# Kernel optimization log

Measured on AMD Instinct MI355X. Metric: run time of the kernel, lower is better.

## Reference

```python
import jax, jax.numpy as jnp
import numpy as np

N, IN, H, OUT = 8192, 128, 256, 128

def _xavier(key, shape):
    lim = float(np.sqrt(6.0 / (shape[0] + shape[1])))
    return jax.random.uniform(key, shape, jnp.float32, -lim, lim)

def setup_inputs() -> dict:
    key = jax.random.key(0)
    ks = jax.random.split(key, 9)
    x = jax.random.normal(ks[0], (N, IN), jnp.float32)
    weighted_adj = jax.random.uniform(ks[1], (N, N), jnp.float32)  # positive edge weights
    W1 = _xavier(ks[2], (IN, H))
    W2 = _xavier(ks[3], (H, H))
    W3 = _xavier(ks[4], (H, OUT))
    q = jax.random.normal(ks[5], (OUT, 1), jnp.float32)
    Wl = _xavier(ks[6], (OUT, OUT))  # nn.Linear weight [out, in]
    bl = jnp.zeros((OUT,), jnp.float32)  # nn.Linear bias (torch default init omitted; zeros)
    b = jax.random.normal(ks[7], (1,), jnp.float32)
    return {"x": x, "weighted_adj": weighted_adj, "W1": W1, "W2": W2, "W3": W3,
            "Wl": Wl, "bl": bl, "q": q, "b": b}

def reference(x, weighted_adj, W1, W2, W3, Wl, bl, q, b):
    # D^{-1/2} A D^{-1/2}: broadcast row/col scaling instead of diag matmuls (same math)
    d_inv_sqrt = jnp.sum(weighted_adj, axis=1) ** -0.5  # [N]
    nadj = d_inv_sqrt[:, None] * weighted_adj * d_inv_sqrt[None, :]  # [N, N]
    # 3 stacked GCN layers (normalized adj is identical each layer)
    h = jax.nn.relu(nadj @ (x @ W1))   # [N, H]
    h = jax.nn.relu(nadj @ (h @ W2))   # [N, H]
    z_context = nadj @ (h @ W3)        # [N, OUT]
    # attention pooling: softmax(tanh(z W^T + b_l) q + b) over nodes
    attn_scores = jnp.tanh(z_context @ Wl.T + bl) @ q + b  # [N, 1]
    attn = jax.nn.softmax(attn_scores, axis=0)
    global_context = jnp.sum(attn * z_context, axis=0)  # [OUT]
    return (z_context, global_context)
```

## Files before the change

kernel.cpp:

```cpp
#include <hip/hip_runtime.h>

typedef unsigned short u16;
typedef unsigned int   u32;
typedef __bf16 bf16x8 __attribute__((ext_vector_type(8)));
typedef float  f32x16 __attribute__((ext_vector_type(16)));

__device__ __forceinline__ u16 f2bf(float f){
  u32 u = __float_as_uint(f);
  u32 r = (u + 0x7FFFu + ((u >> 16) & 1u)) >> 16;
  return (u16)r;
}


__global__ __launch_bounds__(1024) void rowsum_tileA(
    const float* __restrict__ A, u16* __restrict__ Ab, float* __restrict__ ds){
  __shared__ u16 lt[8192];
  const int t = threadIdx.x;
  const int r = t >> 5, q = t & 31;
  const int rg = blockIdx.x;
  const float* ar = A + ((size_t)rg * 32 + r) * 8192;
  float s = 0.f;
  for (int ch = 0; ch < 32; ++ch){
    #pragma unroll
    for (int j = 0; j < 2; ++j){
      const int c4 = ch * 64 + j * 32 + q;
      float4 v = ((const float4*)ar)[c4];
      s += (v.x + v.y) + (v.z + v.w);
      const int cl = (j * 32 + q) * 4;
      const int tile = cl >> 4;
      const int tl   = (r | (((cl >> 3) & 1) << 5)) ^ (tile & 7);
      const int idx  = tile * 512 + tl * 8 + (cl & 7);
      ushort4 o;
      o.x = f2bf(v.x); o.y = f2bf(v.y); o.z = f2bf(v.z); o.w = f2bf(v.w);
      *(ushort4*)(lt + idx) = o;
    }
    __syncthreads();
    {
      const int tile = t >> 6, tl = t & 63;
      uint4 v = *(const uint4*)(lt + tile * 512 + (tl ^ (tile & 7)) * 8);
      uint4* dst = (uint4*)(Ab + ((size_t)rg * 512 + ch * 16) * 512);
      dst[t] = v;
    }
    __syncthreads();
  }
  #pragma unroll
  for (int m = 16; m > 0; m >>= 1) s += __shfl_xor(s, m, 64);
  if (q == 0) ds[rg * 32 + r] = rsqrtf(s);
}

template<int K, int F>
__global__ __launch_bounds__(256) void small_gemm(
    const float* __restrict__ inp, const float* __restrict__ W,
    const float* __restrict__ ds, u16* __restrict__ Vt){
  constexpr int RPB = 16;
  __shared__ float xs[RPB * K];
  const int t  = threadIdx.x;
  const int r0 = blockIdx.x * RPB;
  const float* ip = inp + (size_t)r0 * K;
  constexpr int IT = (RPB * K) / (256 * 4);
  #pragma unroll
  for (int j = 0; j < IT; ++j){
    int c = j * 256 + t;
    ((float4*)xs)[c] = ((const float4*)ip)[c];
  }
  __syncthreads();
  const int o = t % F;
  float acc[16];
  #pragma unroll
  for (int r = 0; r < 16; ++r) acc[r] = 0.f;
  for (int k = 0; k < K; k += 4){
    float w0 = W[(k+0)*F + o];
    float w1 = W[(k+1)*F + o];
    float w2 = W[(k+2)*F + o];
    float w3 = W[(k+3)*F + o];
    #pragma unroll
    for (int r = 0; r < 16; ++r){
      float4 xv = *(const float4*)(xs + r*K + k);
      acc[r] += xv.x*w0 + xv.y*w1 + xv.z*w2 + xv.w*w3;
    }
  }
  const int rb = r0;
  union { u16 u[16]; uint4 v[2]; } pk;
  #pragma unroll
  for (int r = 0; r < 16; ++r) pk.u[r] = f2bf(acc[r] * ds[rb + r]);
  const size_t tile = ((size_t)(o >> 5) * 512 + (rb >> 4)) * 512;
  uint4* dst = (uint4*)(Vt + tile + (size_t)(o & 31) * 8);
  dst[0]  = pk.v[0];
  dst[32] = pk.v[1];
}

__global__ __launch_bounds__(64) void prep_w(
    const float* __restrict__ W2, const float* __restrict__ W3,
    u16* __restrict__ W2t, u16* __restrict__ W3t){
  const int b = blockIdx.x, l = threadIdx.x;
  const float* W; u16* Wt; int F, fi;
  if (b < 128){ W = W2; Wt = W2t; F = 256; fi = b; }
  else        { W = W3; Wt = W3t; F = 128; fi = b - 128; }
  const int CT = F / 32;
  const int kt = fi / CT, ct = fi % CT;
  const int o  = ct * 32 + (l & 31);
  const int kb = kt * 16 + (l >> 5) * 8;
  union { u16 u[8]; uint4 v; } pk;
  #pragma unroll
  for (int e = 0; e < 8; ++e) pk.u[e] = f2bf(W[(size_t)(kb + e) * F + o]);
  *(uint4*)(Wt + (size_t)fi * 512 + l * 8) = pk.v;
}

template<int F>
__global__ __launch_bounds__(256) void small_mfma(
    const u16* __restrict__ Ht, const u16* __restrict__ Wt,
    const float* __restrict__ ds, u16* __restrict__ Vt){
  constexpr int CT = F / 128;
  const int t = threadIdx.x, w = t >> 6, lane = t & 63;
  const int rowt = blockIdx.x;
  const u16* ha = Ht + ((size_t)rowt * 16) * 512 + lane * 8;
  const u16* wb = Wt + ((size_t)(w * CT)) * 512 + lane * 8;
  f32x16 acc[CT];
  #pragma unroll
  for (int ct = 0; ct < CT; ++ct)
    #pragma unroll
    for (int i = 0; i < 16; ++i) acc[ct][i] = 0.f;
  #pragma unroll
  for (int kt = 0; kt < 16; ++kt){
    bf16x8 a = *(const bf16x8*)(const void*)(ha + (size_t)kt * 512);
    #pragma unroll
    for (int ct = 0; ct < CT; ++ct){
      bf16x8 b = *(const bf16x8*)(const void*)(wb + (size_t)(kt * (F/32) + ct) * 512);
      acc[ct] = __builtin_amdgcn_mfma_f32_32x32x16_bf16(a, b, acc[ct], 0, 0, 0);
    }
  }
  const int rhi = (lane >> 5) << 2, cl = lane & 31;
  #pragma unroll
  for (int ct = 0; ct < CT; ++ct){
    const size_t obase = ((size_t)(w * CT + ct) * 512 + rowt * 2) * 512;
    #pragma unroll
    for (int r = 0; r < 16; ++r){
      const int rl = (r & 3) + ((r >> 2) << 3) + rhi;
      const int i  = rowt * 32 + rl;
      const u16 v = f2bf(acc[ct][r] * ds[i]);
      Vt[obase + (size_t)(rl >> 4) * 512 + (cl | (((rl >> 3) & 1) << 5)) * 8 + (rl & 7)] = v;
    }
  }
}

__global__ __launch_bounds__(256) void gemm_rt(
    const u16* __restrict__ Ab, const u16* __restrict__ Vt,
    const float* __restrict__ ds, u16* __restrict__ Hout){
  __shared__ u16 Ls[2][32 * 512];
  const int t = threadIdx.x, w = t >> 6, lane = t & 63;
  const int rowg = blockIdx.x & 127;
  const int colg = blockIdx.x >> 7;

  const u16* sP0 = Ab + ((size_t)(rowg * 2 + 0) * 512) * 512 + lane * 8;
  const u16* sP1 = Ab + ((size_t)(rowg * 2 + 1) * 512) * 512 + lane * 8;
  const u16* sP2 = Vt + ((size_t)(colg * 2 + 0) * 512) * 512 + lane * 8;
  const u16* sP3 = Vt + ((size_t)(colg * 2 + 1) * 512) * 512 + lane * 8;

  f32x16 a00, a01, a10, a11;
  #pragma unroll
  for (int i = 0; i < 16; ++i){ a00[i]=0.f; a01[i]=0.f; a10[i]=0.f; a11[i]=0.f; }

  auto stage = [&](int buf, int c){
    u16* L = &Ls[buf][0] + lane * 8;
    #pragma unroll
    for (int h = 0; h < 2; ++h){
      const int kt = c * 8 + h * 4 + w;
      const int sl = h * 4 + w;
      const size_t so = (size_t)kt * 512;
      __builtin_amdgcn_global_load_lds(
        (const __attribute__((address_space(1))) u32*)(sP0 + so),
        (__attribute__((address_space(3))) u32*)(L + (0  + sl) * 512), 16, 0, 0);
      __builtin_amdgcn_global_load_lds(
        (const __attribute__((address_space(1))) u32*)(sP1 + so),
        (__attribute__((address_space(3))) u32*)(L + (8  + sl) * 512), 16, 0, 0);
      __builtin_amdgcn_global_load_lds(
        (const __attribute__((address_space(1))) u32*)(sP2 + so),
        (__attribute__((address_space(3))) u32*)(L + (16 + sl) * 512), 16, 0, 0);
      __builtin_amdgcn_global_load_lds(
        (const __attribute__((address_space(1))) u32*)(sP3 + so),
        (__attribute__((address_space(3))) u32*)(L + (24 + sl) * 512), 16, 0, 0);
    }
  };
  auto compute = [&](int buf){
    const u16* L = &Ls[buf][0] + lane * 8;
    #pragma unroll
    for (int h = 0; h < 2; ++h){
      const int sl = h * 4 + w;
      bf16x8 fa0 = *(const bf16x8*)(const void*)(L + (0  + sl) * 512);
      bf16x8 fa1 = *(const bf16x8*)(const void*)(L + (8  + sl) * 512);
      bf16x8 fb0 = *(const bf16x8*)(const void*)(L + (16 + sl) * 512);
      bf16x8 fb1 = *(const bf16x8*)(const void*)(L + (24 + sl) * 512);
      a00 = __builtin_amdgcn_mfma_f32_32x32x16_bf16(fa0, fb0, a00, 0, 0, 0);
      a01 = __builtin_amdgcn_mfma_f32_32x32x16_bf16(fa0, fb1, a01, 0, 0, 0);
      a10 = __builtin_amdgcn_mfma_f32_32x32x16_bf16(fa1, fb0, a10, 0, 0, 0);
      a11 = __builtin_amdgcn_mfma_f32_32x32x16_bf16(fa1, fb1, a11, 0, 0, 0);
    }
  };

  stage(0, 0);
  __syncthreads();
  for (int c = 0; c < 64; ++c){
    if (c < 63) stage((c + 1) & 1, c + 1);
    compute(c & 1);
    __syncthreads();
  }

  float* Rf = (float*)(&Ls[0][0]);
  f32x16 aq[4];
  aq[0] = a00; aq[1] = a01; aq[2] = a10; aq[3] = a11;
  if (w >= 2){
    float* o = Rf + (w - 2) * 4096 + lane;
    #pragma unroll
    for (int q = 0; q < 4; ++q)
      #pragma unroll
      for (int r = 0; r < 16; ++r)
        o[(q * 16 + r) * 64] = aq[q][r];
  }
  __syncthreads();
  if (w < 2){
    const float* o = Rf + w * 4096 + lane;
    #pragma unroll
    for (int q = 0; q < 4; ++q)
      #pragma unroll
      for (int r = 0; r < 16; ++r)
        aq[q][r] += o[(q * 16 + r) * 64];
  }
  __syncthreads();
  if (w == 1){
    float* o = Rf + lane;
    #pragma unroll
    for (int q = 0; q < 4; ++q)
      #pragma unroll
      for (int r = 0; r < 16; ++r)
        o[(q * 16 + r) * 64] = aq[q][r];
  }
  __syncthreads();
  if (w == 0){
    const float* o = Rf + lane;
    const int rhi = (lane >> 5) << 2;
    const int cl  = lane & 31;
    #pragma unroll
    for (int q = 0; q < 4; ++q){
      const int rowtile = rowg * 2 + (q >> 1);
      const int ct16    = colg * 4 + (q & 1) * 2 + (cl >> 4);
      #pragma unroll
      for (int r = 0; r < 16; ++r){
        const int rl = (r & 3) + ((r >> 2) << 3) + rhi;
        const int row = rowg * 64 + (q >> 1) * 32 + rl;
        float v = aq[q][r] + o[(q * 16 + r) * 64];
        v *= ds[row];
        v = fmaxf(v, 0.f);
        Hout[((size_t)rowtile * 16 + ct16) * 512
             + (rl | (((cl >> 3) & 1) << 5)) * 8 + (cl & 7)] = f2bf(v);
      }
    }
  }
}

__global__ __launch_bounds__(256) void gemm_rt128(
    const u16* __restrict__ Ab, const u16* __restrict__ Vt,
    const float* __restrict__ ds, float* __restrict__ Fout){
  __shared__ u16 Ls[2][24 * 512];
  const int t = threadIdx.x, w = t >> 6, lane = t & 63;
  const int rowg = blockIdx.x & 255;
  const int colg = blockIdx.x >> 8;

  const u16* sA  = Ab + ((size_t)rowg * 512) * 512 + lane * 8;
  const u16* sB0 = Vt + ((size_t)(colg * 2 + 0) * 512) * 512 + lane * 8;
  const u16* sB1 = Vt + ((size_t)(colg * 2 + 1) * 512) * 512 + lane * 8;

  f32x16 p0, p1;
  #pragma unroll
  for (int i = 0; i < 16; ++i){ p0[i] = 0.f; p1[i] = 0.f; }

  auto stage = [&](int buf, int c){
    u16* L = &Ls[buf][0] + lane * 8;
    #pragma unroll
    for (int h = 0; h < 2; ++h){
      const int kt = c * 8 + h * 4 + w;
      const int sl = h * 4 + w;
      const size_t so = (size_t)kt * 512;
      __builtin_amdgcn_global_load_lds(
        (const __attribute__((address_space(1))) u32*)(sA + so),
        (__attribute__((address_space(3))) u32*)(L + (0  + sl) * 512), 16, 0, 0);
      __builtin_amdgcn_global_load_lds(
        (const __attribute__((address_space(1))) u32*)(sB0 + so),
        (__attribute__((address_space(3))) u32*)(L + (8  + sl) * 512), 16, 0, 0);
      __builtin_amdgcn_global_load_lds(
        (const __attribute__((address_space(1))) u32*)(sB1 + so),
        (__attribute__((address_space(3))) u32*)(L + (16 + sl) * 512), 16, 0, 0);
    }
  };
  auto compute = [&](int buf){
    const u16* L = &Ls[buf][0] + lane * 8;
    #pragma unroll
    for (int h = 0; h < 2; ++h){
      const int sl = h * 4 + w;
      bf16x8 fa  = *(const bf16x8*)(const void*)(L + (0  + sl) * 512);
      bf16x8 fb0 = *(const bf16x8*)(const void*)(L + (8  + sl) * 512);
      bf16x8 fb1 = *(const bf16x8*)(const void*)(L + (16 + sl) * 512);
      p0 = __builtin_amdgcn_mfma_f32_32x32x16_bf16(fa, fb0, p0, 0, 0, 0);
      p1 = __builtin_amdgcn_mfma_f32_32x32x16_bf16(fa, fb1, p1, 0, 0, 0);
    }
  };

  stage(0, 0);
  __syncthreads();
  for (int c = 0; c < 64; ++c){
    if (c < 63) stage((c + 1) & 1, c + 1);
    compute(c & 1);
    __syncthreads();
  }

  float* Rf = (float*)(&Ls[0][0]);
  f32x16 aq[2];
  aq[0] = p0; aq[1] = p1;
  if (w >= 2){
    float* o = Rf + (w - 2) * 2048 + lane;
    #pragma unroll
    for (int q = 0; q < 2; ++q)
      #pragma unroll
      for (int r = 0; r < 16; ++r)
        o[(q * 16 + r) * 64] = aq[q][r];
  }
  __syncthreads();
  if (w < 2){
    const float* o = Rf + w * 2048 + lane;
    #pragma unroll
    for (int q = 0; q < 2; ++q)
      #pragma unroll
      for (int r = 0; r < 16; ++r)
        aq[q][r] += o[(q * 16 + r) * 64];
  }
  __syncthreads();
  if (w == 1){
    float* o = Rf + lane;
    #pragma unroll
    for (int q = 0; q < 2; ++q)
      #pragma unroll
      for (int r = 0; r < 16; ++r)
        o[(q * 16 + r) * 64] = aq[q][r];
  }
  __syncthreads();
  if (w == 0){
    const float* o = Rf + lane;
    const int rhi = (lane >> 5) << 2;
    const int cl  = lane & 31;
    #pragma unroll
    for (int q = 0; q < 2; ++q){
      const int cbase = colg * 64 + q * 32;
      #pragma unroll
      for (int r = 0; r < 16; ++r){
        const int rl = (r & 3) + ((r >> 2) << 3) + rhi;
        const int row = rowg * 32 + rl;
        float v = aq[q][r] + o[(q * 16 + r) * 64];
        Fout[(size_t)row * 128 + cbase + cl] = v * ds[row];
      }
    }
  }
}

__device__ __forceinline__ float tanh_fast(float x){
  x = fminf(fmaxf(x, -15.f), 15.f);
  float e = __expf(2.f * x);
  return (e - 1.f) / (e + 1.f);
}

__global__ __launch_bounds__(256) void attn_scores(
    const float* __restrict__ Z, const float* __restrict__ Wl,
    const float* __restrict__ bl, const float* __restrict__ q,
    const float* __restrict__ bsc, float* __restrict__ sc){
  __shared__ float wl[128 * 128];
  const int t = threadIdx.x, lane = t & 63, wave = t >> 6;
  for (int j = 0; j < 64; ++j){
    int idx = j * 256 + t;
    int o = idx >> 7, k = idx & 127;
    int c = k >> 2, e = k & 3;
    wl[o * 128 + (((c ^ (o & 31)) << 2) | e)] = Wl[idx];
  }
  __syncthreads();
  const float bl0 = bl[lane], bl1 = bl[lane + 64];
  const float q0  = q[lane],  q1  = q[lane + 64];
  const float bb  = bsc[0];
  const int r0 = blockIdx.x * 16;
  for (int rr = 0; rr < 4; ++rr){
    int r = r0 + wave * 4 + rr;
    float d0 = 0.f, d1 = 0.f;
    #pragma unroll
    for (int c = 0; c < 32; ++c){
      float4 zv = *(const float4*)(Z + (size_t)r * 128 + c * 4);
      float4 w0 = *(const float4*)&wl[ lane      * 128 + ((c ^ (lane & 31)) << 2)];
      float4 w1 = *(const float4*)&wl[(lane + 64)* 128 + ((c ^ (lane & 31)) << 2)];
      d0 += zv.x*w0.x + zv.y*w0.y + zv.z*w0.z + zv.w*w0.w;
      d1 += zv.x*w1.x + zv.y*w1.y + zv.z*w1.z + zv.w*w1.w;
    }
    float s = tanh_fast(d0 + bl0) * q0 + tanh_fast(d1 + bl1) * q1;
    #pragma unroll
    for (int off = 32; off > 0; off >>= 1) s += __shfl_down(s, off, 64);
    if (lane == 0) sc[r] = s + bb;
  }
}

__global__ __launch_bounds__(1024) void softmax_red(
    const float* __restrict__ sc, float* __restrict__ sred){
  const int t = threadIdx.x, lane = t & 63, wave = t >> 6;
  __shared__ float red[16];
  float m = -1e30f;
  for (int i = t; i < 8192; i += 1024) m = fmaxf(m, sc[i]);
  #pragma unroll
  for (int off = 32; off > 0; off >>= 1) m = fmaxf(m, __shfl_down(m, off, 64));
  if (lane == 0) red[wave] = m;
  __syncthreads();
  if (t == 0){
    float mm = red[0];
    for (int w = 1; w < 16; ++w) mm = fmaxf(mm, red[w]);
    red[0] = mm;
  }
  __syncthreads();
  const float bmax = red[0];
  __syncthreads();
  float s = 0.f;
  for (int i = t; i < 8192; i += 1024) s += __expf(sc[i] - bmax);
  #pragma unroll
  for (int off = 32; off > 0; off >>= 1) s += __shfl_down(s, off, 64);
  if (lane == 0) red[wave] = s;
  __syncthreads();
  if (t == 0){
    float ss = 0.f;
    for (int w = 0; w < 16; ++w) ss += red[w];
    sred[0] = bmax; sred[1] = ss;
  }
}

__global__ __launch_bounds__(256) void weighted_part(
    const float* __restrict__ sc, const float* __restrict__ sred,
    const float* __restrict__ Z, float* __restrict__ part){
  const int blk = blockIdx.x, t = threadIdx.x;
  const int o = t & 127, h = t >> 7;
  const float bmax = sred[0], inv = 1.f / sred[1];
  float acc = 0.f;
  const int i0 = blk * 128;
  for (int i = i0 + h; i < i0 + 128; i += 2){
    float w = __expf(sc[i] - bmax) * inv;
    acc += w * Z[(size_t)i * 128 + o];
  }
  __shared__ float l[256];
  l[t] = acc;
  __syncthreads();
  if (h == 0) part[blk * 128 + o] = l[o] + l[o + 128];
}

__global__ __launch_bounds__(128) void final_red(
    const float* __restrict__ part, float* __restrict__ out){
  const int o = threadIdx.x;
  float s = 0.f;
  for (int b = 0; b < 64; ++b) s += part[b * 128 + o];
  out[o] = s;
}

extern "C" void kernel_launch(void* const* d_in, const int* in_sizes, int n_in,
                              void* d_out, int out_size, void* d_ws, size_t ws_size,
                              hipStream_t stream){
  const float* x  = (const float*)d_in[0];
  const float* A  = (const float*)d_in[1];
  const float* W1 = (const float*)d_in[2];
  const float* W2 = (const float*)d_in[3];
  const float* W3 = (const float*)d_in[4];
  const float* Wl = (const float*)d_in[5];
  const float* bl = (const float*)d_in[6];
  const float* q  = (const float*)d_in[7];
  const float* b  = (const float*)d_in[8];
  float* out = (float*)d_out;
  char* ws = (char*)d_ws;

  u16*   AB   = (u16*)(ws);
  float* DS   = (float*)(ws + 134217728);
  u16*   VT   = (u16*)(ws + 134250496);
  u16*   HB   = (u16*)(ws + 138444800);
  float* SC   = (float*)(ws + 142639104);
  float* SP   = (float*)(ws + 142671872);
  float* SRED = (float*)(ws + 142704640);
  u16*   W2T  = (u16*)(ws + 142705664);
  u16*   W3T  = (u16*)(ws + 142836736);

  rowsum_tileA<<<256, 1024, 0, stream>>>(A, AB, DS);
  prep_w<<<192, 64, 0, stream>>>(W2, W3, W2T, W3T);
  small_gemm<128, 256><<<512, 256, 0, stream>>>(x, W1, DS, VT);
  gemm_rt<<<512, 256, 0, stream>>>(AB, VT, DS, HB);
  small_mfma<256><<<256, 256, 0, stream>>>(HB, W2T, DS, VT);
  gemm_rt<<<512, 256, 0, stream>>>(AB, VT, DS, HB);
  small_mfma<128><<<256, 256, 0, stream>>>(HB, W3T, DS, VT);
  gemm_rt128<<<512, 256, 0, stream>>>(AB, VT, DS, out);
  attn_scores<<<512, 256, 0, stream>>>(out, Wl, bl, q, b, SC);
  softmax_red<<<1, 1024, 0, stream>>>(SC, SRED);
  weighted_part<<<64, 256, 0, stream>>>(SC, SRED, out, SP);
  final_red<<<1, 128, 0, stream>>>(SP, out + 8192 * 128);
}
```

Measured before the change: 307.9 us.

## Use MFMA for first layer x@W1 and double-buffer LDS in rowsum_tileA

The scalar fp32 small_gemm for x@W1 is replaced by a bf16 pack of x (prep_x), a tiled pack of W1 added to prep_w, and the existing MFMA small_mfma kernel templated on K-tile count. The rowsum_tileA kernel double-buffers its LDS staging tile so the second barrier per chunk can be dropped. This trades one fp32 layer for bf16 precision and adds a kernel launch. The main cost it targets is the scalar FMA work and the per-chunk barrier stall.

```diff
diff --git a/kernel.cpp b/kernel.cpp
--- a/kernel.cpp
+++ b/kernel.cpp
@@ -14,13 +14,14 @@
 
 __global__ __launch_bounds__(1024) void rowsum_tileA(
     const float* __restrict__ A, u16* __restrict__ Ab, float* __restrict__ ds){
-  __shared__ u16 lt[8192];
+  __shared__ u16 lt[2][8192];
   const int t = threadIdx.x;
   const int r = t >> 5, q = t & 31;
   const int rg = blockIdx.x;
   const float* ar = A + ((size_t)rg * 32 + r) * 8192;
   float s = 0.f;
   for (int ch = 0; ch < 32; ++ch){
+    u16* lb = lt[ch & 1];
     #pragma unroll
     for (int j = 0; j < 2; ++j){
       const int c4 = ch * 64 + j * 32 + q;
@@ -32,70 +33,51 @@
       const int idx  = tile * 512 + tl * 8 + (cl & 7);
       ushort4 o;
       o.x = f2bf(v.x); o.y = f2bf(v.y); o.z = f2bf(v.z); o.w = f2bf(v.w);
-      *(ushort4*)(lt + idx) = o;
+      *(ushort4*)(lb + idx) = o;
     }
     __syncthreads();
     {
       const int tile = t >> 6, tl = t & 63;
-      uint4 v = *(const uint4*)(lt + tile * 512 + (tl ^ (tile & 7)) * 8);
+      uint4 v = *(const uint4*)(lb + tile * 512 + (tl ^ (tile & 7)) * 8);
       uint4* dst = (uint4*)(Ab + ((size_t)rg * 512 + ch * 16) * 512);
       dst[t] = v;
     }
-    __syncthreads();
   }
   #pragma unroll
   for (int m = 16; m > 0; m >>= 1) s += __shfl_xor(s, m, 64);
   if (q == 0) ds[rg * 32 + r] = rsqrtf(s);
 }
 
-template<int K, int F>
-__global__ __launch_bounds__(256) void small_gemm(
-    const float* __restrict__ inp, const float* __restrict__ W,
-    const float* __restrict__ ds, u16* __restrict__ Vt){
-  constexpr int RPB = 16;
-  __shared__ float xs[RPB * K];
-  const int t  = threadIdx.x;
-  const int r0 = blockIdx.x * RPB;
-  const float* ip = inp + (size_t)r0 * K;
-  constexpr int IT = (RPB * K) / (256 * 4);
-  #pragma unroll
-  for (int j = 0; j < IT; ++j){
-    int c = j * 256 + t;
-    ((float4*)xs)[c] = ((const float4*)ip)[c];
-  }
-  __syncthreads();
-  const int o = t % F;
-  float acc[16];
-  #pragma unroll
-  for (int r = 0; r < 16; ++r) acc[r] = 0.f;
-  for (int k = 0; k < K; k += 4){
-    float w0 = W[(k+0)*F + o];
-    float w1 = W[(k+1)*F + o];
-    float w2 = W[(k+2)*F + o];
-    float w3 = W[(k+3)*F + o];
-    #pragma unroll
-    for (int r = 0; r < 16; ++r){
-      float4 xv = *(const float4*)(xs + r*K + k);
-      acc[r] += xv.x*w0 + xv.y*w1 + xv.z*w2 + xv.w*w3;
-    }
-  }
-  const int rb = r0;
-  union { u16 u[16]; uint4 v[2]; } pk;
-  #pragma unroll
-  for (int r = 0; r < 16; ++r) pk.u[r] = f2bf(acc[r] * ds[rb + r]);
-  const size_t tile = ((size_t)(o >> 5) * 512 + (rb >> 4)) * 512;
-  uint4* dst = (uint4*)(Vt + tile + (size_t)(o & 31) * 8);
-  dst[0]  = pk.v[0];
-  dst[32] = pk.v[1];
+__global__ __launch_bounds__(1024) void prep_x(
+    const float* __restrict__ x, u16* __restrict__ Xt){
+  __shared__ u16 lt[4096];
+  const int t = threadIdx.x;
+  const int r = t >> 5, q = t & 31;
+  const int rg = blockIdx.x;
+  float4 v = ((const float4*)(x + ((size_t)rg * 32 + r) * 128))[q];
+  const int cl = q * 4;
+  const int tile = cl >> 4;
+  const int tl   = (r | (((cl >> 3) & 1) << 5)) ^ (tile & 7);
+  ushort4 o;
+  o.x = f2bf(v.x); o.y = f2bf(v.y); o.z = f2bf(v.z); o.w = f2bf(v.w);
+  *(ushort4*)(lt + tile * 512 + tl * 8 + (cl & 7)) = o;
+  __syncthreads();
+  if (t < 512){
+    const int tile2 = t >> 6, tl2 = t & 63;
+    uint4 w = *(const uint4*)(lt + tile2 * 512 + (tl2 ^ (tile2 & 7)) * 8);
+    ((uint4*)(Xt + (size_t)rg * 4096))[t] = w;
+  }
 }
 
 __global__ __launch_bounds__(64) void prep_w(
-    const float* __restrict__ W2, const float* __restrict__ W3,
+    const float* __restrict__ W1, const float* __restrict__ W2,
+    const float* __restrict__ W3, u16* __restrict__ W1t,
     u16* __restrict__ W2t, u16* __restrict__ W3t){
   const int b = blockIdx.x, l = threadIdx.x;
   const float* W; u16* Wt; int F, fi;
-  if (b < 128){ W = W2; Wt = W2t; F = 256; fi = b; }
-  else        { W = W3; Wt = W3t; F = 128; fi = b - 128; }
+  if (b < 64)       { W = W1; Wt = W1t; F = 256; fi = b; }
+  else if (b < 192) { W = W2; Wt = W2t; F = 256; fi = b - 64; }
+  else              { W = W3; Wt = W3t; F = 128; fi = b - 192; }
   const int CT = F / 32;
   const int kt = fi / CT, ct = fi % CT;
   const int o  = ct * 32 + (l & 31);
@@ -106,14 +88,14 @@
   *(uint4*)(Wt + (size_t)fi * 512 + l * 8) = pk.v;
 }
 
-template<int F>
+template<int F, int KT>
 __global__ __launch_bounds__(256) void small_mfma(
     const u16* __restrict__ Ht, const u16* __restrict__ Wt,
     const float* __restrict__ ds, u16* __restrict__ Vt){
   constexpr int CT = F / 128;
   const int t = threadIdx.x, w = t >> 6, lane = t & 63;
   const int rowt = blockIdx.x;
-  const u16* ha = Ht + ((size_t)rowt * 16) * 512 + lane * 8;
+  const u16* ha = Ht + ((size_t)rowt * KT) * 512 + lane * 8;
   const u16* wb = Wt + ((size_t)(w * CT)) * 512 + lane * 8;
   f32x16 acc[CT];
   #pragma unroll
@@ -121,7 +103,7 @@
     #pragma unroll
     for (int i = 0; i < 16; ++i) acc[ct][i] = 0.f;
   #pragma unroll
-  for (int kt = 0; kt < 16; ++kt){
+  for (int kt = 0; kt < KT; ++kt){
     bf16x8 a = *(const bf16x8*)(const void*)(ha + (size_t)kt * 512);
     #pragma unroll
     for (int ct = 0; ct < CT; ++ct){
@@ -482,14 +464,17 @@
   float* SRED = (float*)(ws + 142704640);
   u16*   W2T  = (u16*)(ws + 142705664);
   u16*   W3T  = (u16*)(ws + 142836736);
+  u16*   W1T  = (u16*)(ws + 142902272);
+  u16*   XT   = (u16*)(ws + 142967808);
 
   rowsum_tileA<<<256, 1024, 0, stream>>>(A, AB, DS);
-  prep_w<<<192, 64, 0, stream>>>(W2, W3, W2T, W3T);
-  small_gemm<128, 256><<<512, 256, 0, stream>>>(x, W1, DS, VT);
+  prep_x<<<256, 1024, 0, stream>>>(x, XT);
+  prep_w<<<256, 64, 0, stream>>>(W1, W2, W3, W1T, W2T, W3T);
+  small_mfma<256, 8><<<256, 256, 0, stream>>>(XT, W1T, DS, VT);
   gemm_rt<<<512, 256, 0, stream>>>(AB, VT, DS, HB);
-  small_mfma<256><<<256, 256, 0, stream>>>(HB, W2T, DS, VT);
+  small_mfma<256, 16><<<256, 256, 0, stream>>>(HB, W2T, DS, VT);
   gemm_rt<<<512, 256, 0, stream>>>(AB, VT, DS, HB);
-  small_mfma<128><<<256, 256, 0, stream>>>(HB, W3T, DS, VT);
+  small_mfma<128, 16><<<256, 256, 0, stream>>>(HB, W3T, DS, VT);
   gemm_rt128<<<512, 256, 0, stream>>>(AB, VT, DS, out);
   attn_scores<<<512, 256, 0, stream>>>(out, Wl, bl, q, b, SC);
   softmax_red<<<1, 1024, 0, stream>>>(SC, SRED);
```

New measurement: 288.5 us (median of 2 runs). 1.07x faster.
